# Kernel optimization log

Hardware: AMD Instinct MI355X
Metric: run time of the kernel (lower is better)

Reference implementation:

```python
import jax, jax.numpy as jnp
import numpy as np

PC = 512      # proposal_channels == conv_channels
INCH = 512    # in_channels of branch
B = 8
T = 64        # pyramid level length (feat_t) at order=0
TF = 256      # frame_level_feature length (clip_length)
KERNELS = [8, 16, 8, 4, 2, 2, 2]  # ConPoolingKernal
CLC = 498     # feature_lastclass channels (CLC + 2 == 500)
GROUPS = 32


def _gn(x, gamma, beta):
    # GroupNorm(32, C) over [B, C, L]
    Bb, C, L = x.shape
    xg = x.reshape(Bb, GROUPS, C // GROUPS, L)
    m = xg.mean(axis=(2, 3), keepdims=True)
    v = xg.var(axis=(2, 3), keepdims=True)
    xn = ((xg - m) * jax.lax.rsqrt(v + 1e-5)).reshape(Bb, C, L)
    return xn * gamma[None, :, None] + beta[None, :, None]


def _c1(x, w, b):
    # Unit1D kernel_shape=1: pointwise conv
    return jnp.einsum('bct,oc->bot', x, w) + b[None, :, None]


def _bmp(feat, segs):
    # BoundaryMaxPooling: first C/2 channels max-pooled over segs[...,0:2],
    # second C/2 over segs[...,2:4] (inclusive integer ranges, clamped).
    Bb, C, L = feat.shape
    C2 = C // 2
    pos = jnp.arange(L)
    def pool(f, s, e):
        s = jnp.clip(s, 0, L - 1)
        e = jnp.maximum(jnp.clip(e, 0, L - 1), s)
        mask = (pos[None, None, :] >= s[..., None]) & (pos[None, None, :] <= e[..., None])  # [B,T,L]
        return jnp.max(jnp.where(mask[:, None], f[:, :, None, :], -jnp.inf), axis=-1)  # [B,C2,T]
    return jnp.concatenate([pool(feat[:, :C2], segs[..., 0], segs[..., 1]),
                            pool(feat[:, C2:], segs[..., 2], segs[..., 3])], axis=1)


def _anchor_gather(feat, anc, K):
    # Vectorized per-anchor clamp/slice + nearest F.interpolate(size=K):
    # src index for output k of a slice [l, r] is l + floor(k * (r - l + 1) / K).
    Bb, C, L = feat.shape
    left = jnp.clip(anc[..., 0], 0, L)
    right = jnp.clip(anc[..., 1], 0, L)
    valid = right > left                      # empty slices -> zeros (torch branch)
    seglen = right + 1 - left
    k = jnp.arange(K)
    idx = jnp.clip(left[..., None] + (k[None, None, :] * seglen[..., None]) // K, 0, L - 1)  # [B,T,K]
    g = jax.vmap(lambda f, ix: f[:, ix])(feat, idx)   # [B,C,T,K]
    return g * valid[:, None, :, None].astype(feat.dtype)


def setup_inputs() -> dict:
    key = jax.random.key(0)
    ks = jax.random.split(key, 16)
    f32 = jnp.float32
    s = 0.02
    def w(k, shape):
        return jax.random.normal(k, shape, f32) * s
    inp = {}
    inp['feature'] = jax.random.normal(ks[0], (B, INCH, T), f32)
    inp['frame_level_feature'] = jax.random.normal(ks[1], (B, PC, TF), f32)
    inp['segments'] = jax.random.randint(ks[2], (B, T, 4), 0, T).astype(jnp.int32)
    inp['frame_segments'] = jax.random.randint(ks[3], (B, T, 4), 0, TF).astype(jnp.int32)
    inp['feature_lastclass'] = jax.random.normal(ks[4], (B, CLC, T), f32)
    inp['anchor'] = jnp.sort(jax.random.randint(ks[5], (B, T, 2), 0, T), axis=-1).astype(jnp.int32)
    inp['frame_anchor'] = jnp.sort(jax.random.randint(ks[6], (B, T, 2), 0, TF), axis=-1).astype(jnp.int32)
    inp['order'] = 0
    inp['LocResult_feature'] = jax.random.normal(ks[7], (B, 2, T), f32)
    inp['w_cur'] = w(ks[8], (PC, INCH)); inp['b_cur'] = jnp.zeros((PC,), f32)
    inp['g_cur'] = jnp.ones((PC,), f32); inp['be_cur'] = jnp.zeros((PC,), f32)
    inp['w_lr'] = w(ks[9], (2 * PC, INCH)); inp['b_lr'] = jnp.zeros((2 * PC,), f32)
    inp['g_lr'] = jnp.ones((2 * PC,), f32); inp['be_lr'] = jnp.zeros((2 * PC,), f32)
    inp['w_roi'] = w(ks[10], (PC, PC)); inp['b_roi'] = jnp.zeros((PC,), f32)
    inp['g_roi'] = jnp.ones((PC,), f32); inp['be_roi'] = jnp.zeros((PC,), f32)
    K1 = KERNELS[1]; K0 = KERNELS[0]
    inp['w_cp'] = w(ks[11], (PC, 2 * PC, K1)); inp['b_cp'] = jnp.zeros((PC,), f32)
    inp['w_cp0'] = w(ks[12], (PC, PC, K0)); inp['b_cp0'] = jnp.zeros((PC,), f32)
    CIN = 6 * PC + 500
    inp['w_prop'] = w(ks[13], (INCH, CIN)); inp['b_prop'] = jnp.zeros((INCH,), f32)
    inp['g_prop'] = jnp.ones((INCH,), f32); inp['be_prop'] = jnp.zeros((INCH,), f32)
    return inp


def reference(feature, frame_level_feature, segments, frame_segments, feature_lastclass,
              anchor, frame_anchor, order, LocResult_feature,
              w_cur, b_cur, g_cur, be_cur, w_lr, b_lr, g_lr, be_lr,
              w_roi, b_roi, g_roi, be_roi, w_cp, b_cp, w_cp0, b_cp0,
              w_prop, b_prop, g_prop, be_prop):
    relu = jax.nn.relu
    fm_short = relu(_gn(_c1(feature, w_cur, b_cur), g_cur, be_cur))           # [B,PC,T]
    feat_lr = relu(_gn(_c1(feature, w_lr, b_lr), g_lr, be_lr))                # [B,2PC,T]
    prop_feature = _bmp(feat_lr, segments)                                    # [B,2PC,T]
    prop_roi = relu(_gn(_c1(_bmp(frame_level_feature, frame_segments), w_roi, b_roi), g_roi, be_roi))
    K1 = KERNELS[order + 1]
    K0 = KERNELS[0]
    g1 = _anchor_gather(feat_lr, anchor, K1)                                  # [B,2PC,T,K1]
    con_feature = jnp.einsum('bctk,ock->bot', g1, w_cp) + b_cp[None, :, None]  # valid conv K1->1
    g0 = _anchor_gather(frame_level_feature, frame_anchor, K0)                # [B,PC,T,K0]
    frame_con = jnp.einsum('bctk,ock->bot', g0, w_cp0) + b_cp0[None, :, None]
    prop_con = relu(_gn(_c1(frame_con, w_roi, b_roi), g_roi, be_roi))
    cat = jnp.concatenate([prop_roi, prop_feature, fm_short, feature_lastclass,
                           con_feature, prop_con, LocResult_feature], axis=1)  # [B,6PC+500,T]
    out = relu(_gn(_c1(cat, w_prop, b_prop), g_prop, be_prop))                # [B,INCH,T]
    return (out, feat_lr)
```

## Files before the change

kernel.cpp:

```cpp
#include <hip/hip_runtime.h>
#include <math.h>

#define BB 8
#define CATP 3584
#define CAT_REAL 3572

typedef __attribute__((ext_vector_type(8))) short short8;
typedef __attribute__((ext_vector_type(4))) float f32x4;

__device__ inline ushort f2bf(float f) {
  union { float f; unsigned u; } x;
  x.f = f;
  return (ushort)((x.u + 0x7FFFu + ((x.u >> 16) & 1u)) >> 16);
}
__device__ inline float bf2f(unsigned us) {
  union { unsigned u; float f; } x;
  x.u = us << 16;
  return x.f;
}

template <int Cin, int Kf>
__device__ void cpT_tile(const float* __restrict__ W, ushort* __restrict__ D,
                         int nt, int cc) {
  const int tid = threadIdx.x;
  const int j = tid >> 6, l4 = (tid >> 4) & 3, l15 = tid & 15;
  const int o = nt * 64 + j * 16 + l15;
  const int cb = cc * 32 + l4 * 8;
  ushort rg[8][Kf];
#pragma unroll
  for (int q = 0; q < 8; q++) {
    const float* row = W + ((size_t)o * Cin + cb + q) * Kf;
#pragma unroll
    for (int kq = 0; kq < Kf / 4; kq++) {
      const float4 f = *(const float4*)(row + kq * 4);
      rg[q][kq * 4 + 0] = f2bf(f.x);
      rg[q][kq * 4 + 1] = f2bf(f.y);
      rg[q][kq * 4 + 2] = f2bf(f.z);
      rg[q][kq * 4 + 3] = f2bf(f.w);
    }
  }
#pragma unroll
  for (int k = 0; k < Kf; k++) {
    uint4 pk;
    pk.x = (unsigned)rg[0][k] | ((unsigned)rg[1][k] << 16);
    pk.y = (unsigned)rg[2][k] | ((unsigned)rg[3][k] << 16);
    pk.z = (unsigned)rg[4][k] | ((unsigned)rg[5][k] << 16);
    pk.w = (unsigned)rg[6][k] | ((unsigned)rg[7][k] << 16);
    *(uint4*)(D + ((size_t)(nt * Kf + k) * (Cin >> 5) + cc) * 2048 + tid * 8) = pk;
  }
}

__global__ __launch_bounds__(256) void prep_kernel(
    const float* __restrict__ w_cur, const float* __restrict__ w_lr,
    const float* __restrict__ w_roi, const float* __restrict__ w_prop,
    ushort* __restrict__ Wcomb, ushort* __restrict__ Wroi,
    ushort* __restrict__ Wprop, const float* __restrict__ w_cp,
    ushort* __restrict__ WcpT, const float* __restrict__ w_cp0,
    ushort* __restrict__ Wcp0T, const float* __restrict__ feature,
    const float* __restrict__ frame_feat, const float* __restrict__ lastcls,
    const float* __restrict__ locres, ushort* __restrict__ Ft,
    ushort* __restrict__ FfT, ushort* __restrict__ cat) {
  __shared__ float tile[64 * 65];
  const int bid = blockIdx.x;
  if (bid < 1408) {
    const int i = bid * 256 + threadIdx.x;
    const float* src;
    ushort* dst;
    int o, k8, Kc;
    bool pad = false;
    if (i < 98304) {
      o = i >> 6; k8 = i & 63; Kc = 16;
      src = (o < 512) ? (w_cur + (size_t)o * 512)
                      : (w_lr + (size_t)(o - 512) * 512);
      dst = Wcomb;
    } else if (i < 131072) {
      const int r = i - 98304;
      o = r >> 6; k8 = r & 63; Kc = 16;
      src = w_roi + (size_t)o * 512;
      dst = Wroi;
    } else {
      const int r = i - 131072;
      if (r >= 229376) return;
      o = r / 448; k8 = r % 448; Kc = 112;
      src = w_prop + (size_t)o * CAT_REAL;
      dst = Wprop;
      pad = true;
    }
    const int k = k8 * 8;
    float v[8];
    if (pad) {
#pragma unroll
      for (int q = 0; q < 8; q++) v[q] = (k + q < CAT_REAL) ? src[k + q] : 0.f;
    } else {
      const float4 f0 = *(const float4*)(src + k);
      const float4 f1 = *(const float4*)(src + k + 4);
      v[0] = f0.x; v[1] = f0.y; v[2] = f0.z; v[3] = f0.w;
      v[4] = f1.x; v[5] = f1.y; v[6] = f1.z; v[7] = f1.w;
    }
    uint4 pk;
    pk.x = (unsigned)f2bf(v[0]) | ((unsigned)f2bf(v[1]) << 16);
    pk.y = (unsigned)f2bf(v[2]) | ((unsigned)f2bf(v[3]) << 16);
    pk.z = (unsigned)f2bf(v[4]) | ((unsigned)f2bf(v[5]) << 16);
    pk.w = (unsigned)f2bf(v[6]) | ((unsigned)f2bf(v[7]) << 16);
    const int ot = o >> 6, ii = (o >> 4) & 3, l15 = o & 15;
    const int kc = k8 >> 2, l4 = k8 & 3;
    const size_t flat =
        ((((size_t)ot * Kc + kc) * 4 + ii) * 64 + l4 * 16 + l15) * 8;
    *(uint4*)(dst + flat) = pk;
    return;
  }
  if (bid < 1792) {
    const int local = bid - 1408;
    if (local < 256)
      cpT_tile<1024, 16>(w_cp, WcpT, local >> 5, local & 31);
    else {
      const int r = local - 256;
      cpT_tile<512, 8>(w_cp0, Wcp0T, r >> 4, r & 15);
    }
    return;
  }
  const int local = bid - 1792;
  const float* src;
  ushort* dst;
  int Cr, Cw, L, rs, co, cblk, lblk, b;
  if (local < 64) {
    src = feature; dst = Ft; Cr = 512; Cw = 512; L = 64; rs = 512; co = 0;
    cblk = local & 7; lblk = 0; b = local >> 3;
  } else if (local < 320) {
    const int r = local - 64;
    src = frame_feat; dst = FfT; Cr = 512; Cw = 512; L = 256; rs = 512; co = 0;
    cblk = r & 7; lblk = (r >> 3) & 3; b = r >> 5;
  } else if (local < 384) {
    const int r = local - 320;
    src = lastcls; dst = cat; Cr = 498; Cw = 498; L = 64; rs = CATP; co = 2048;
    cblk = r & 7; lblk = 0; b = r >> 3;
  } else {
    const int r = local - 384;
    src = locres; dst = cat; Cr = 2; Cw = 14; L = 64; rs = CATP; co = 3570;
    cblk = 0; lblk = 0; b = r;
  }
  const int c0 = cblk * 64, l0 = lblk * 64;
  for (int e = threadIdx.x; e < 4096; e += 256) {
    const int cc = e >> 6, ll = e & 63;
    const int c = c0 + cc;
    tile[cc * 65 + ll] = (c < Cr) ? src[((size_t)b * Cr + c) * L + l0 + ll] : 0.f;
  }
  __syncthreads();
  for (int e = threadIdx.x; e < 4096; e += 256) {
    const int ll = e >> 6, cc = e & 63;
    const int c = c0 + cc;
    if (c < Cw)
      dst[((size_t)b * L + l0 + ll) * rs + co + c] = f2bf(tile[cc * 65 + ll]);
  }
}

__global__ __launch_bounds__(256) void gemm_gn_seg_kernel(
    int nblk0,
    const ushort* __restrict__ X0, const ushort* __restrict__ W0,
    const float* __restrict__ b0, const float* __restrict__ g0,
    const float* __restrict__ e0, int Kp0, int cs0, float* of0, int om0,
    ushort* co0, int cst0, int coff0,
    const ushort* __restrict__ X1, const ushort* __restrict__ W1,
    const float* __restrict__ b1, const float* __restrict__ g1,
    const float* __restrict__ e1, int Kp1, int cs1, float* of1, int om1,
    ushort* co1, int cst1, int coff1) {
  const int bx = blockIdx.x;
  const bool s1 = bx >= nblk0;
  const ushort* Xt = s1 ? X1 : X0;
  const ushort* Wb = s1 ? W1 : W0;
  const float* bias = s1 ? b1 : b0;
  const float* gamma = s1 ? g1 : g0;
  const float* beta = s1 ? e1 : e0;
  const int Kp = s1 ? Kp1 : Kp0;
  const int cpgShift = s1 ? cs1 : cs0;
  float* outF = s1 ? of1 : of0;
  const int outFM = s1 ? om1 : om0;
  ushort* catOut = s1 ? co1 : co0;
  const int catStride = s1 ? cst1 : cst0;
  const int chOff = s1 ? coff1 : coff0;
  const int o0 = (s1 ? bx - nblk0 : bx) * 64;

  const int b = blockIdx.y;
  const int w = threadIdx.x >> 6;
  const int lane = threadIdx.x & 63;
  const int l15 = lane & 15, l4 = lane >> 4;
  const int wk = Kp >> 2;
  const int kbeg = w * wk, kend = kbeg + wk;

  f32x4 acc[4][4] = {};
  const ushort* wbase = Wb + (size_t)(o0 >> 6) * (Kp >> 5) * 2048 + lane * 8;
  const ushort* bp[4];
#pragma unroll
  for (int j = 0; j < 4; j++)
    bp[j] = Xt + (size_t)(b * 64 + j * 16 + l15) * Kp + l4 * 8;

  for (int k = kbeg; k < kend; k += 32) {
    const int kc = k >> 5;
    short8 a[4], x[4];
#pragma unroll
    for (int i = 0; i < 4; i++)
      a[i] = *(const short8*)(wbase + ((size_t)kc * 4 + i) * 512);
#pragma unroll
    for (int j = 0; j < 4; j++) x[j] = *(const short8*)(bp[j] + k);
#pragma unroll
    for (int i = 0; i < 4; i++)
#pragma unroll
      for (int j = 0; j < 4; j++)
        acc[i][j] = __builtin_amdgcn_mfma_f32_16x16x32_bf16(a[i], x[j],
                                                            acc[i][j], 0, 0, 0);
  }

  __shared__ float red[64 * 65];
  for (int ww = 0; ww < 4; ww++) {
    __syncthreads();
    if (w == ww) {
#pragma unroll
      for (int i = 0; i < 4; i++)
#pragma unroll
        for (int j = 0; j < 4; j++)
#pragma unroll
          for (int r = 0; r < 4; r++) {
            const int m = i * 16 + l4 * 4 + r;
            const int n = j * 16 + l15;
            if (ww == 0)
              red[m * 65 + n] = acc[i][j][r] + bias[o0 + m];
            else
              red[m * 65 + n] += acc[i][j][r];
          }
    }
  }
  __syncthreads();

  const int cpg = 1 << cpgShift;
  const int ngroups = 64 >> cpgShift;
  __shared__ float rs[4], rss[4], gmean[4], grstd[4];
  for (int gi = 0; gi < ngroups; gi++) {
    float s = 0.f, ss = 0.f;
    const int nel = cpg << 6;
    for (int e = threadIdx.x; e < nel; e += 256) {
      const float v = red[((gi << cpgShift) + (e >> 6)) * 65 + (e & 63)];
      s += v;
      ss += v * v;
    }
#pragma unroll
    for (int off = 32; off > 0; off >>= 1) {
      s += __shfl_down(s, off);
      ss += __shfl_down(ss, off);
    }
    if (lane == 0) { rs[w] = s; rss[w] = ss; }
    __syncthreads();
    if (threadIdx.x == 0) {
      const float ts = rs[0] + rs[1] + rs[2] + rs[3];
      const float tss = rss[0] + rss[1] + rss[2] + rss[3];
      const float mean = ts / (float)nel;
      const float var = tss / (float)nel - mean * mean;
      gmean[gi] = mean;
      grstd[gi] = rsqrtf(var + 1e-5f);
    }
    __syncthreads();
  }

  if (outF) {
    for (int e = threadIdx.x; e < 4096; e += 256) {
      const int m = e >> 6, n = e & 63;
      const int gi = m >> cpgShift;
      const int c = o0 + m;
      float v = (red[m * 65 + n] - gmean[gi]) * grstd[gi] * gamma[c] + beta[c];
      v = fmaxf(v, 0.f);
      outF[((size_t)b * outFM + c) * 64 + n] = v;
    }
  }
  if (catOut) {
    for (int e = threadIdx.x; e < 4096; e += 256) {
      const int n = e >> 6, m = e & 63;
      const int gi = m >> cpgShift;
      const int c = o0 + m;
      float v = (red[m * 65 + n] - gmean[gi]) * grstd[gi] * gamma[c] + beta[c];
      v = fmaxf(v, 0.f);
      catOut[((size_t)(b * 64) + n) * catStride + chOff + c] = f2bf(v);
    }
  }
}

__global__ __launch_bounds__(256) void gemm_part_kernel(
    const ushort* __restrict__ Xt, const ushort* __restrict__ Wb,
    float* __restrict__ P) {
  const int ot = blockIdx.x;
  const int b = blockIdx.y;
  const int kz = blockIdx.z;
  const int w = threadIdx.x >> 6;
  const int lane = threadIdx.x & 63;
  const int l15 = lane & 15, l4 = lane >> 4;
  const int kbeg = kz * 896 + w * 224;
  const int kend = kbeg + 224;

  f32x4 acc[4][4] = {};
  const ushort* wbase = Wb + (size_t)ot * (CATP >> 5) * 2048 + lane * 8;
  const ushort* bp[4];
#pragma unroll
  for (int j = 0; j < 4; j++)
    bp[j] = Xt + (size_t)(b * 64 + j * 16 + l15) * CATP + l4 * 8;

  for (int k = kbeg; k < kend; k += 32) {
    const int kc = k >> 5;
    short8 a[4], x[4];
#pragma unroll
    for (int i = 0; i < 4; i++)
      a[i] = *(const short8*)(wbase + ((size_t)kc * 4 + i) * 512);
#pragma unroll
    for (int j = 0; j < 4; j++) x[j] = *(const short8*)(bp[j] + k);
#pragma unroll
    for (int i = 0; i < 4; i++)
#pragma unroll
      for (int j = 0; j < 4; j++)
        acc[i][j] = __builtin_amdgcn_mfma_f32_16x16x32_bf16(a[i], x[j],
                                                            acc[i][j], 0, 0, 0);
  }

  __shared__ float red[64 * 65];
  for (int ww = 0; ww < 4; ww++) {
    __syncthreads();
    if (w == ww) {
#pragma unroll
      for (int i = 0; i < 4; i++)
#pragma unroll
        for (int j = 0; j < 4; j++)
#pragma unroll
          for (int r = 0; r < 4; r++) {
            const int m = i * 16 + l4 * 4 + r;
            const int n = j * 16 + l15;
            if (ww == 0)
              red[m * 65 + n] = acc[i][j][r];
            else
              red[m * 65 + n] += acc[i][j][r];
          }
    }
  }
  __syncthreads();
  float* Pp = P + (((size_t)kz * BB + b) * 512 + ot * 64) * 64;
  for (int e = threadIdx.x; e < 4096; e += 256) Pp[e] = red[(e >> 6) * 65 + (e & 63)];
}

__global__ __launch_bounds__(256) void reduce_gn_kernel(
    const float* __restrict__ P, const float* __restrict__ bias,
    const float* __restrict__ gamma, const float* __restrict__ beta,
    float* __restrict__ outF) {
  const int ot = blockIdx.x;
  const int b = blockIdx.y;
  const int o0 = ot * 64;
  const int w = threadIdx.x >> 6;
  const int lane = threadIdx.x & 63;
  __shared__ float red[64 * 65];
  for (int e = threadIdx.x; e < 4096; e += 256) {
    const int m = e >> 6, n = e & 63;
    float s = bias[o0 + m];
#pragma unroll
    for (int z = 0; z < 4; z++)
      s += P[(((size_t)z * BB + b) * 512 + o0 + m) * 64 + n];
    red[m * 65 + n] = s;
  }
  __syncthreads();
  __shared__ float rs[4], rss[4], gmean[4], grstd[4];
  for (int gi = 0; gi < 4; gi++) {
    float s = 0.f, ss = 0.f;
    for (int e = threadIdx.x; e < 1024; e += 256) {
      const float v = red[((gi << 4) + (e >> 6)) * 65 + (e & 63)];
      s += v;
      ss += v * v;
    }
#pragma unroll
    for (int off = 32; off > 0; off >>= 1) {
      s += __shfl_down(s, off);
      ss += __shfl_down(ss, off);
    }
    if (lane == 0) { rs[w] = s; rss[w] = ss; }
    __syncthreads();
    if (threadIdx.x == 0) {
      const float ts = rs[0] + rs[1] + rs[2] + rs[3];
      const float tss = rss[0] + rss[1] + rss[2] + rss[3];
      const float mean = ts / 1024.f;
      const float var = tss / 1024.f - mean * mean;
      gmean[gi] = mean;
      grstd[gi] = rsqrtf(var + 1e-5f);
    }
    __syncthreads();
  }
  for (int e = threadIdx.x; e < 4096; e += 256) {
    const int m = e >> 6, n = e & 63;
    const int gi = m >> 4;
    const int c = o0 + m;
    float v = (red[m * 65 + n] - gmean[gi]) * grstd[gi] * gamma[c] + beta[c];
    outF[((size_t)b * 512 + c) * 64 + n] = fmaxf(v, 0.f);
  }
}

template <int C, int L>
__device__ void bmp_body(const ushort* __restrict__ Xt,
                         const int* __restrict__ segs, ushort* __restrict__ Y,
                         int rowStride, int chOff, float2 (*pmax)[512]) {
  constexpr int C2 = C / 2;
  constexpr int P2 = C2 / 2;
  constexpr int CH = P2 / 64;
  const int t = blockIdx.x;
  const int b = blockIdx.y;
  const int w = threadIdx.x >> 6;
  const int lane = threadIdx.x & 63;
  const int* sg = segs + ((size_t)b * 64 + t) * 4;
  const ushort* Xb = Xt + (size_t)b * L * C;
#pragma unroll
  for (int h = 0; h < 2; h++) {
    const int s = min(max(sg[2 * h], 0), L - 1);
    const int e = max(min(max(sg[2 * h + 1], 0), L - 1), s);
#pragma unroll
    for (int q = 0; q < CH; q++) {
      const int p = q * 64 + lane;
      const ushort* base = Xb + h * C2 + 2 * p;
      float a0 = -INFINITY, a1 = -INFINITY;
      float c0 = -INFINITY, c1 = -INFINITY;
      int l = s + w;
      for (; l + 4 <= e; l += 8) {
        const unsigned u0 = *(const unsigned*)(base + (size_t)l * C);
        const unsigned u1 = *(const unsigned*)(base + (size_t)(l + 4) * C);
        a0 = fmaxf(a0, bf2f(u0 & 0xffffu));
        a1 = fmaxf(a1, bf2f(u0 >> 16));
        c0 = fmaxf(c0, bf2f(u1 & 0xffffu));
        c1 = fmaxf(c1, bf2f(u1 >> 16));
      }
      if (l <= e) {
        const unsigned u0 = *(const unsigned*)(base + (size_t)l * C);
        a0 = fmaxf(a0, bf2f(u0 & 0xffffu));
        a1 = fmaxf(a1, bf2f(u0 >> 16));
      }
      pmax[w][h * P2 + p] = make_float2(fmaxf(a0, c0), fmaxf(a1, c1));
    }
  }
  __syncthreads();
  for (int idx = threadIdx.x; idx < 2 * P2; idx += 256) {
    float2 m = pmax[0][idx];
#pragma unroll
    for (int ww = 1; ww < 4; ww++) {
      const float2 v = pmax[ww][idx];
      m.x = fmaxf(m.x, v.x);
      m.y = fmaxf(m.y, v.y);
    }
    const unsigned o = (unsigned)f2bf(m.x) | ((unsigned)f2bf(m.y) << 16);
    *(unsigned*)(Y + ((size_t)(b * 64) + t) * rowStride + chOff + 2 * idx) = o;
  }
}

__global__ __launch_bounds__(256) void bmp_dual_kernel(
    const ushort* __restrict__ FlrT, const int* __restrict__ segments,
    ushort* __restrict__ cat, const ushort* __restrict__ FfT,
    const int* __restrict__ frame_segs, ushort* __restrict__ XbmpT) {
  __shared__ float2 pm[4][512];
  if (blockIdx.z == 0)
    bmp_body<1024, 64>(FlrT, segments, cat, CATP, 512, pm);
  else
    bmp_body<512, 256>(FfT, frame_segs, XbmpT, 512, 0, pm);
}

template <int Kf, int L, int Cin>
__device__ void anchor_mfma_body(const ushort* __restrict__ src,
                                 const int* __restrict__ anc,
                                 const ushort* __restrict__ Wt,
                                 float* __restrict__ P, int slice, float* red) {
  const int nt = blockIdx.x;
  const int b = blockIdx.y;
  const int w = threadIdx.x >> 6;
  const int lane = threadIdx.x & 63;
  const int l15 = lane & 15, l4 = lane >> 4;
  const int kz = slice >> 1, chalf = slice & 1;
  const int k = kz * 4 + w;
  const int cbase = chalf * (Cin / 2);

  const ushort* rp[4];
#pragma unroll
  for (int i = 0; i < 4; i++) {
    const int t = i * 16 + l15;
    const int a0 = anc[((size_t)b * 64 + t) * 2 + 0];
    const int a1 = anc[((size_t)b * 64 + t) * 2 + 1];
    const int left = min(max(a0, 0), L);
    const int right = min(max(a1, 0), L);
    const int seglen = right + 1 - left;
    const int ix = min(max(left + (k * seglen) / Kf, 0), L - 1);
    rp[i] = src + ((size_t)b * L + ix) * Cin + cbase + l4 * 8;
  }
  const ushort* wb = Wt + (size_t)(nt * Kf + k) * (Cin >> 5) * 2048 + lane * 8;

  f32x4 acc[4][4] = {};
  for (int c0 = 0; c0 < Cin / 2; c0 += 32) {
    const int cc = (cbase + c0) >> 5;
    short8 a[4], bb[4];
#pragma unroll
    for (int i = 0; i < 4; i++) a[i] = *(const short8*)(rp[i] + c0);
#pragma unroll
    for (int j = 0; j < 4; j++)
      bb[j] = *(const short8*)(wb + ((size_t)cc * 4 + j) * 512);
#pragma unroll
    for (int i = 0; i < 4; i++)
#pragma unroll
      for (int j = 0; j < 4; j++)
        acc[i][j] = __builtin_amdgcn_mfma_f32_16x16x32_bf16(a[i], bb[j],
                                                            acc[i][j], 0, 0, 0);
  }

  for (int ww = 0; ww < 4; ww++) {
    __syncthreads();
    if (w == ww) {
#pragma unroll
      for (int i = 0; i < 4; i++)
#pragma unroll
        for (int j = 0; j < 4; j++)
#pragma unroll
          for (int r = 0; r < 4; r++) {
            const int m = i * 16 + l4 * 4 + r;
            const int n = j * 16 + l15;
            if (ww == 0)
              red[m * 65 + n] = acc[i][j][r];
            else
              red[m * 65 + n] += acc[i][j][r];
          }
    }
  }
  __syncthreads();
  float* Pp = P + (((size_t)slice * BB + b) * 512 + nt * 64) * 64;
  for (int e = threadIdx.x; e < 4096; e += 256) {
    const int n = e >> 6, m = e & 63;
    Pp[e] = red[m * 65 + n];
  }
}

__global__ __launch_bounds__(256) void anchor_mfma_dual_kernel(
    const ushort* __restrict__ FlrT, const int* __restrict__ anchor,
    const ushort* __restrict__ WcpT, float* __restrict__ P1,
    const ushort* __restrict__ FfT, const int* __restrict__ frame_anchor,
    const ushort* __restrict__ Wcp0T, float* __restrict__ P0) {
  __shared__ float red[64 * 65];
  const int z = blockIdx.z;
  if (z < 8)
    anchor_mfma_body<16, 64, 1024>(FlrT, anchor, WcpT, P1, z, red);
  else
    anchor_mfma_body<8, 256, 512>(FfT, frame_anchor, Wcp0T, P0, z - 8, red);
}

__device__ void anchor_reduce_body(const float* __restrict__ P, int ks,
                                   const float* __restrict__ bias,
                                   const int* __restrict__ anc, int L,
                                   ushort* __restrict__ Y, int rowStride,
                                   int chOff, float* tile, float* sval) {
  const int o0 = blockIdx.x * 64;
  const int b = blockIdx.y;
  if (threadIdx.x < 64) {
    const int t = threadIdx.x;
    const int a0 = anc[((size_t)b * 64 + t) * 2 + 0];
    const int a1 = anc[((size_t)b * 64 + t) * 2 + 1];
    const int left = min(max(a0, 0), L);
    const int right = min(max(a1, 0), L);
    sval[t] = (right > left) ? 1.f : 0.f;
  }
  __syncthreads();
  for (int e = threadIdx.x; e < 4096; e += 256) {
    const int nl = e >> 6, m = e & 63;
    const int n = o0 + nl;
    float s = 0.f;
    for (int z = 0; z < ks; z++)
      s += P[(((size_t)z * BB + b) * 512 + n) * 64 + m];
    tile[nl * 65 + m] = s * sval[m] + bias[n];
  }
  __syncthreads();
  for (int e = threadIdx.x; e < 4096; e += 256) {
    const int m = e >> 6, nl = e & 63;
    Y[((size_t)(b * 64) + m) * rowStride + chOff + o0 + nl] =
        f2bf(tile[nl * 65 + m]);
  }
}

__global__ __launch_bounds__(256) void anchor_reduce_dual_kernel(
    const float* __restrict__ P1, const float* __restrict__ b_cp,
    const int* __restrict__ anchor, ushort* __restrict__ cat,
    const float* __restrict__ P0, const float* __restrict__ b_cp0,
    const int* __restrict__ frame_anchor, ushort* __restrict__ FconT) {
  __shared__ float tile[64 * 65];
  __shared__ float sval[64];
  if (blockIdx.z == 0)
    anchor_reduce_body(P1, 8, b_cp, anchor, 64, cat, CATP, 2546, tile, sval);
  else
    anchor_reduce_body(P0, 4, b_cp0, frame_anchor, 256, FconT, 512, 0, tile, sval);
}

extern "C" void kernel_launch(void* const* d_in, const int* in_sizes, int n_in,
                              void* d_out, int out_size, void* d_ws,
                              size_t ws_size, hipStream_t stream) {
  const float* feature      = (const float*)d_in[0];
  const float* frame_feat   = (const float*)d_in[1];
  const int*   segments     = (const int*)d_in[2];
  const int*   frame_segs   = (const int*)d_in[3];
  const float* feat_lastcls = (const float*)d_in[4];
  const int*   anchor       = (const int*)d_in[5];
  const int*   frame_anchor = (const int*)d_in[6];
  const float* locres       = (const float*)d_in[8];
  const float* w_cur  = (const float*)d_in[9];
  const float* b_cur  = (const float*)d_in[10];
  const float* g_cur  = (const float*)d_in[11];
  const float* be_cur = (const float*)d_in[12];
  const float* w_lr   = (const float*)d_in[13];
  const float* b_lr   = (const float*)d_in[14];
  const float* g_lr   = (const float*)d_in[15];
  const float* be_lr  = (const float*)d_in[16];
  const float* w_roi  = (const float*)d_in[17];
  const float* b_roi  = (const float*)d_in[18];
  const float* g_roi  = (const float*)d_in[19];
  const float* be_roi = (const float*)d_in[20];
  const float* w_cp   = (const float*)d_in[21];
  const float* b_cp   = (const float*)d_in[22];
  const float* w_cp0  = (const float*)d_in[23];
  const float* b_cp0  = (const float*)d_in[24];
  const float* w_prop = (const float*)d_in[25];
  const float* b_prop = (const float*)d_in[26];
  const float* g_prop = (const float*)d_in[27];
  const float* be_prop= (const float*)d_in[28];

  float* out_main = (float*)d_out;
  float* feat_lr  = (float*)d_out + BB * 512 * 64;

  ushort* cat_t  = (ushort*)d_ws;
  ushort* Ft     = cat_t + 1835008;
  ushort* XbmpT  = Ft + 262144;
  ushort* FconT  = XbmpT + 262144;
  ushort* Wcomb  = FconT + 262144;
  ushort* Wroi   = Wcomb + 786432;
  ushort* Wprop  = Wroi + 262144;
  ushort* WcpT   = Wprop + 1835008;
  ushort* Wcp0T  = WcpT + 8388608;
  ushort* FlrT   = Wcp0T + 2097152;
  ushort* FfT    = FlrT + 524288;
  float*  P1     = (float*)(FfT + 1048576);
  float*  P0     = P1 + 2097152;
  float*  P9     = P0 + 1048576;

  prep_kernel<<<2184, 256, 0, stream>>>(
      w_cur, w_lr, w_roi, w_prop, Wcomb, Wroi, Wprop, w_cp, WcpT, w_cp0,
      Wcp0T, feature, frame_feat, feat_lastcls, locres, Ft, FfT, cat_t);

  gemm_gn_seg_kernel<<<dim3(24, BB), 256, 0, stream>>>(
      8,
      Ft, Wcomb, b_cur, g_cur, be_cur, 512, 4, nullptr, 0, cat_t, CATP, 1536,
      Ft, Wcomb + 512 * 512, b_lr, g_lr, be_lr, 512, 5, feat_lr, 1024, FlrT,
      1024, 0);

  bmp_dual_kernel<<<dim3(64, BB, 2), 256, 0, stream>>>(
      FlrT, segments, cat_t, FfT, frame_segs, XbmpT);

  anchor_mfma_dual_kernel<<<dim3(8, BB, 12), 256, 0, stream>>>(
      FlrT, anchor, WcpT, P1, FfT, frame_anchor, Wcp0T, P0);

  anchor_reduce_dual_kernel<<<dim3(8, BB, 2), 256, 0, stream>>>(
      P1, b_cp, anchor, cat_t, P0, b_cp0, frame_anchor, FconT);

  gemm_gn_seg_kernel<<<dim3(16, BB), 256, 0, stream>>>(
      8,
      XbmpT, Wroi, b_roi, g_roi, be_roi, 512, 4, nullptr, 0, cat_t, CATP, 0,
      FconT, Wroi, b_roi, g_roi, be_roi, 512, 4, nullptr, 0, cat_t, CATP, 3058);

  gemm_part_kernel<<<dim3(8, BB, 4), 256, 0, stream>>>(cat_t, Wprop, P9);

  reduce_gn_kernel<<<dim3(8, BB), 256, 0, stream>>>(
      P9, b_prop, g_prop, be_prop, out_main);
}
```

Baseline: 271.3 us.

## Regroup pipeline stages into dependency-ordered fused kernels with per-wave output tiling

```diff
diff --git a/kernel.cpp b/kernel.cpp
--- a/kernel.cpp
+++ b/kernel.cpp
@@ -154,86 +154,51 @@
   }
 }
 
-__global__ __launch_bounds__(256) void gemm_gn_seg_kernel(
-    int nblk0,
-    const ushort* __restrict__ X0, const ushort* __restrict__ W0,
-    const float* __restrict__ b0, const float* __restrict__ g0,
-    const float* __restrict__ e0, int Kp0, int cs0, float* of0, int om0,
-    ushort* co0, int cst0, int coff0,
-    const ushort* __restrict__ X1, const ushort* __restrict__ W1,
-    const float* __restrict__ b1, const float* __restrict__ g1,
-    const float* __restrict__ e1, int Kp1, int cs1, float* of1, int om1,
-    ushort* co1, int cst1, int coff1) {
-  const int bx = blockIdx.x;
-  const bool s1 = bx >= nblk0;
-  const ushort* Xt = s1 ? X1 : X0;
-  const ushort* Wb = s1 ? W1 : W0;
-  const float* bias = s1 ? b1 : b0;
-  const float* gamma = s1 ? g1 : g0;
-  const float* beta = s1 ? e1 : e0;
-  const int Kp = s1 ? Kp1 : Kp0;
-  const int cpgShift = s1 ? cs1 : cs0;
-  float* outF = s1 ? of1 : of0;
-  const int outFM = s1 ? om1 : om0;
-  ushort* catOut = s1 ? co1 : co0;
-  const int catStride = s1 ? cst1 : cst0;
-  const int chOff = s1 ? coff1 : coff0;
-  const int o0 = (s1 ? bx - nblk0 : bx) * 64;
-
-  const int b = blockIdx.y;
+__device__ void gemm_gn_body(const ushort* __restrict__ Xt,
+                             const ushort* __restrict__ Wb,
+                             const float* __restrict__ bias,
+                             const float* __restrict__ gamma,
+                             const float* __restrict__ beta, int Kp,
+                             int cpgShift, float* __restrict__ outF, int outFM,
+                             ushort* __restrict__ catOut, int catStride,
+                             int chOff, int ot, int b, float* smem) {
+  float* red = smem;
+  float* rs = smem + 4224;
+  float* rss = smem + 4228;
+  float* gmean = smem + 4232;
+  float* grstd = smem + 4236;
   const int w = threadIdx.x >> 6;
   const int lane = threadIdx.x & 63;
   const int l15 = lane & 15, l4 = lane >> 4;
-  const int wk = Kp >> 2;
-  const int kbeg = w * wk, kend = kbeg + wk;
-
-  f32x4 acc[4][4] = {};
-  const ushort* wbase = Wb + (size_t)(o0 >> 6) * (Kp >> 5) * 2048 + lane * 8;
+  const int o0 = ot * 64;
+
+  f32x4 acc[4] = {};
+  const ushort* wbase = Wb + (size_t)ot * (Kp >> 5) * 2048 + lane * 8;
   const ushort* bp[4];
 #pragma unroll
   for (int j = 0; j < 4; j++)
     bp[j] = Xt + (size_t)(b * 64 + j * 16 + l15) * Kp + l4 * 8;
-
-  for (int k = kbeg; k < kend; k += 32) {
-    const int kc = k >> 5;
-    short8 a[4], x[4];
-#pragma unroll
-    for (int i = 0; i < 4; i++)
-      a[i] = *(const short8*)(wbase + ((size_t)kc * 4 + i) * 512);
-#pragma unroll
-    for (int j = 0; j < 4; j++) x[j] = *(const short8*)(bp[j] + k);
-#pragma unroll
-    for (int i = 0; i < 4; i++)
-#pragma unroll
-      for (int j = 0; j < 4; j++)
-        acc[i][j] = __builtin_amdgcn_mfma_f32_16x16x32_bf16(a[i], x[j],
-                                                            acc[i][j], 0, 0, 0);
-  }
-
-  __shared__ float red[64 * 65];
-  for (int ww = 0; ww < 4; ww++) {
-    __syncthreads();
-    if (w == ww) {
-#pragma unroll
-      for (int i = 0; i < 4; i++)
-#pragma unroll
-        for (int j = 0; j < 4; j++)
-#pragma unroll
-          for (int r = 0; r < 4; r++) {
-            const int m = i * 16 + l4 * 4 + r;
-            const int n = j * 16 + l15;
-            if (ww == 0)
-              red[m * 65 + n] = acc[i][j][r] + bias[o0 + m];
-            else
-              red[m * 65 + n] += acc[i][j][r];
-          }
-    }
-  }
+  const int nkc = Kp >> 5;
+  for (int kc = 0; kc < nkc; kc++) {
+    const short8 a = *(const short8*)(wbase + ((size_t)kc * 4 + w) * 512);
+    short8 x[4];
+#pragma unroll
+    for (int j = 0; j < 4; j++) x[j] = *(const short8*)(bp[j] + kc * 32);
+#pragma unroll
+    for (int j = 0; j < 4; j++)
+      acc[j] = __builtin_amdgcn_mfma_f32_16x16x32_bf16(a, x[j], acc[j], 0, 0, 0);
+  }
+#pragma unroll
+  for (int j = 0; j < 4; j++)
+#pragma unroll
+    for (int r = 0; r < 4; r++) {
+      const int m = w * 16 + l4 * 4 + r;
+      red[m * 65 + j * 16 + l15] = acc[j][r] + bias[o0 + m];
+    }
   __syncthreads();
 
   const int cpg = 1 << cpgShift;
   const int ngroups = 64 >> cpgShift;
-  __shared__ float rs[4], rss[4], gmean[4], grstd[4];
   for (int gi = 0; gi < ngroups; gi++) {
     float s = 0.f, ss = 0.f;
     const int nel = cpg << 6;
@@ -282,63 +247,35 @@
   }
 }
 
-__global__ __launch_bounds__(256) void gemm_part_kernel(
-    const ushort* __restrict__ Xt, const ushort* __restrict__ Wb,
-    float* __restrict__ P) {
-  const int ot = blockIdx.x;
-  const int b = blockIdx.y;
-  const int kz = blockIdx.z;
+__device__ void gemm_part_body(const ushort* __restrict__ Xt,
+                               const ushort* __restrict__ Wb,
+                               float* __restrict__ P, int ot, int b, int slice,
+                               int kbeg, int kend) {
   const int w = threadIdx.x >> 6;
   const int lane = threadIdx.x & 63;
   const int l15 = lane & 15, l4 = lane >> 4;
-  const int kbeg = kz * 896 + w * 224;
-  const int kend = kbeg + 224;
-
-  f32x4 acc[4][4] = {};
+  f32x4 acc[4] = {};
   const ushort* wbase = Wb + (size_t)ot * (CATP >> 5) * 2048 + lane * 8;
   const ushort* bp[4];
 #pragma unroll
   for (int j = 0; j < 4; j++)
     bp[j] = Xt + (size_t)(b * 64 + j * 16 + l15) * CATP + l4 * 8;
-
   for (int k = kbeg; k < kend; k += 32) {
     const int kc = k >> 5;
-    short8 a[4], x[4];
-#pragma unroll
-    for (int i = 0; i < 4; i++)
-      a[i] = *(const short8*)(wbase + ((size_t)kc * 4 + i) * 512);
+    const short8 a = *(const short8*)(wbase + ((size_t)kc * 4 + w) * 512);
+    short8 x[4];
 #pragma unroll
     for (int j = 0; j < 4; j++) x[j] = *(const short8*)(bp[j] + k);
 #pragma unroll
-    for (int i = 0; i < 4; i++)
-#pragma unroll
-      for (int j = 0; j < 4; j++)
-        acc[i][j] = __builtin_amdgcn_mfma_f32_16x16x32_bf16(a[i], x[j],
-                                                            acc[i][j], 0, 0, 0);
-  }
-
-  __shared__ float red[64 * 65];
-  for (int ww = 0; ww < 4; ww++) {
-    __syncthreads();
-    if (w == ww) {
-#pragma unroll
-      for (int i = 0; i < 4; i++)
-#pragma unroll
-        for (int j = 0; j < 4; j++)
-#pragma unroll
-          for (int r = 0; r < 4; r++) {
-            const int m = i * 16 + l4 * 4 + r;
-            const int n = j * 16 + l15;
-            if (ww == 0)
-              red[m * 65 + n] = acc[i][j][r];
-            else
-              red[m * 65 + n] += acc[i][j][r];
-          }
-    }
-  }
-  __syncthreads();
-  float* Pp = P + (((size_t)kz * BB + b) * 512 + ot * 64) * 64;
-  for (int e = threadIdx.x; e < 4096; e += 256) Pp[e] = red[(e >> 6) * 65 + (e & 63)];
+    for (int j = 0; j < 4; j++)
+      acc[j] = __builtin_amdgcn_mfma_f32_16x16x32_bf16(a, x[j], acc[j], 0, 0, 0);
+  }
+  float* Pp = P + (((size_t)slice * BB + b) * 512 + ot * 64) * 64;
+#pragma unroll
+  for (int j = 0; j < 4; j++)
+#pragma unroll
+    for (int r = 0; r < 4; r++)
+      Pp[(w * 16 + l4 * 4 + r) * 64 + j * 16 + l15] = acc[j][r];
 }
 
 __global__ __launch_bounds__(256) void reduce_gn_kernel(
@@ -397,12 +334,11 @@
 template <int C, int L>
 __device__ void bmp_body(const ushort* __restrict__ Xt,
                          const int* __restrict__ segs, ushort* __restrict__ Y,
-                         int rowStride, int chOff, float2 (*pmax)[512]) {
+                         int rowStride, int chOff, int t, int b,
+                         float2 (*pmax)[512]) {
   constexpr int C2 = C / 2;
   constexpr int P2 = C2 / 2;
   constexpr int CH = P2 / 64;
-  const int t = blockIdx.x;
-  const int b = blockIdx.y;
   const int w = threadIdx.x >> 6;
   const int lane = threadIdx.x & 63;
   const int* sg = segs + ((size_t)b * 64 + t) * 4;
@@ -448,108 +384,58 @@
   }
 }
 
-__global__ __launch_bounds__(256) void bmp_dual_kernel(
-    const ushort* __restrict__ FlrT, const int* __restrict__ segments,
-    ushort* __restrict__ cat, const ushort* __restrict__ FfT,
-    const int* __restrict__ frame_segs, ushort* __restrict__ XbmpT) {
-  __shared__ float2 pm[4][512];
-  if (blockIdx.z == 0)
-    bmp_body<1024, 64>(FlrT, segments, cat, CATP, 512, pm);
-  else
-    bmp_body<512, 256>(FfT, frame_segs, XbmpT, 512, 0, pm);
-}
-
-template <int Kf, int L, int Cin>
-__device__ void anchor_mfma_body(const ushort* __restrict__ src,
-                                 const int* __restrict__ anc,
-                                 const ushort* __restrict__ Wt,
-                                 float* __restrict__ P, int slice, float* red) {
-  const int nt = blockIdx.x;
-  const int b = blockIdx.y;
+template <int Kf, int L, int Cin, int NT>
+__device__ void anchor_body2(const ushort* __restrict__ src,
+                             const int* __restrict__ anc,
+                             const ushort* __restrict__ Wt,
+                             float* __restrict__ P, int nt, int b, int slice) {
   const int w = threadIdx.x >> 6;
   const int lane = threadIdx.x & 63;
   const int l15 = lane & 15, l4 = lane >> 4;
-  const int kz = slice >> 1, chalf = slice & 1;
-  const int k = kz * 4 + w;
-  const int cbase = chalf * (Cin / 2);
-
-  const ushort* rp[4];
-#pragma unroll
-  for (int i = 0; i < 4; i++) {
-    const int t = i * 16 + l15;
-    const int a0 = anc[((size_t)b * 64 + t) * 2 + 0];
-    const int a1 = anc[((size_t)b * 64 + t) * 2 + 1];
-    const int left = min(max(a0, 0), L);
-    const int right = min(max(a1, 0), L);
-    const int seglen = right + 1 - left;
+  const int t = w * 16 + l15;
+  const int a0 = anc[((size_t)b * 64 + t) * 2 + 0];
+  const int a1 = anc[((size_t)b * 64 + t) * 2 + 1];
+  const int left = min(max(a0, 0), L);
+  const int right = min(max(a1, 0), L);
+  const int seglen = right + 1 - left;
+
+  f32x4 acc[4] = {};
+#pragma unroll
+  for (int kt = 0; kt < NT; kt++) {
+    const int k = slice * NT + kt;
     const int ix = min(max(left + (k * seglen) / Kf, 0), L - 1);
-    rp[i] = src + ((size_t)b * L + ix) * Cin + cbase + l4 * 8;
-  }
-  const ushort* wb = Wt + (size_t)(nt * Kf + k) * (Cin >> 5) * 2048 + lane * 8;
-
-  f32x4 acc[4][4] = {};
-  for (int c0 = 0; c0 < Cin / 2; c0 += 32) {
-    const int cc = (cbase + c0) >> 5;
-    short8 a[4], bb[4];
-#pragma unroll
-    for (int i = 0; i < 4; i++) a[i] = *(const short8*)(rp[i] + c0);
-#pragma unroll
-    for (int j = 0; j < 4; j++)
-      bb[j] = *(const short8*)(wb + ((size_t)cc * 4 + j) * 512);
-#pragma unroll
-    for (int i = 0; i < 4; i++)
+    const ushort* rp = src + ((size_t)b * L + ix) * Cin + l4 * 8;
+    const ushort* wb = Wt + ((size_t)nt * Kf + k) * (Cin >> 5) * 2048 + lane * 8;
+#pragma unroll 4
+    for (int c0 = 0; c0 < Cin; c0 += 32) {
+      const int cc = c0 >> 5;
+      const short8 a = *(const short8*)(rp + c0);
+      short8 bbf[4];
 #pragma unroll
       for (int j = 0; j < 4; j++)
-        acc[i][j] = __builtin_amdgcn_mfma_f32_16x16x32_bf16(a[i], bb[j],
-                                                            acc[i][j], 0, 0, 0);
-  }
-
-  for (int ww = 0; ww < 4; ww++) {
-    __syncthreads();
-    if (w == ww) {
-#pragma unroll
-      for (int i = 0; i < 4; i++)
-#pragma unroll
-        for (int j = 0; j < 4; j++)
-#pragma unroll
-          for (int r = 0; r < 4; r++) {
-            const int m = i * 16 + l4 * 4 + r;
-            const int n = j * 16 + l15;
-            if (ww == 0)
-              red[m * 65 + n] = acc[i][j][r];
-            else
-              red[m * 65 + n] += acc[i][j][r];
-          }
-    }
-  }
-  __syncthreads();
-  float* Pp = P + (((size_t)slice * BB + b) * 512 + nt * 64) * 64;
-  for (int e = threadIdx.x; e < 4096; e += 256) {
-    const int n = e >> 6, m = e & 63;
-    Pp[e] = red[m * 65 + n];
-  }
-}
-
-__global__ __launch_bounds__(256) void anchor_mfma_dual_kernel(
-    const ushort* __restrict__ FlrT, const int* __restrict__ anchor,
-    const ushort* __restrict__ WcpT, float* __restrict__ P1,
-    const ushort* __restrict__ FfT, const int* __restrict__ frame_anchor,
-    const ushort* __restrict__ Wcp0T, float* __restrict__ P0) {
-  __shared__ float red[64 * 65];
-  const int z = blockIdx.z;
-  if (z < 8)
-    anchor_mfma_body<16, 64, 1024>(FlrT, anchor, WcpT, P1, z, red);
-  else
-    anchor_mfma_body<8, 256, 512>(FfT, frame_anchor, Wcp0T, P0, z - 8, red);
+        bbf[j] = *(const short8*)(wb + ((size_t)cc * 4 + j) * 512);
+#pragma unroll
+      for (int j = 0; j < 4; j++)
+        acc[j] =
+            __builtin_amdgcn_mfma_f32_16x16x32_bf16(a, bbf[j], acc[j], 0, 0, 0);
+    }
+  }
+  float* Pp = P + (((size_t)slice * BB + b) * 64) * 512 + nt * 64;
+#pragma unroll
+  for (int j = 0; j < 4; j++)
+#pragma unroll
+    for (int r = 0; r < 4; r++)
+      Pp[(size_t)(w * 16 + l4 * 4 + r) * 512 + j * 16 + l15] = acc[j][r];
 }
 
 __device__ void anchor_reduce_body(const float* __restrict__ P, int ks,
                                    const float* __restrict__ bias,
                                    const int* __restrict__ anc, int L,
                                    ushort* __restrict__ Y, int rowStride,
-                                   int chOff, float* tile, float* sval) {
-  const int o0 = blockIdx.x * 64;
-  const int b = blockIdx.y;
+                                   int chOff, int ot, int b, float* smem) {
+  float* tile = smem;
+  float* sval = smem + 4160;
+  const int o0 = ot * 64;
   if (threadIdx.x < 64) {
     const int t = threadIdx.x;
     const int a0 = anc[((size_t)b * 64 + t) * 2 + 0];
@@ -560,12 +446,11 @@
   }
   __syncthreads();
   for (int e = threadIdx.x; e < 4096; e += 256) {
-    const int nl = e >> 6, m = e & 63;
-    const int n = o0 + nl;
+    const int m = e >> 6, nl = e & 63;
     float s = 0.f;
     for (int z = 0; z < ks; z++)
-      s += P[(((size_t)z * BB + b) * 512 + n) * 64 + m];
-    tile[nl * 65 + m] = s * sval[m] + bias[n];
+      s += P[(((size_t)z * BB + b) * 64 + m) * 512 + o0 + nl];
+    tile[nl * 65 + m] = s * sval[m] + bias[o0 + nl];
   }
   __syncthreads();
   for (int e = threadIdx.x; e < 4096; e += 256) {
@@ -575,17 +460,96 @@
   }
 }
 
-__global__ __launch_bounds__(256) void anchor_reduce_dual_kernel(
-    const float* __restrict__ P1, const float* __restrict__ b_cp,
-    const int* __restrict__ anchor, ushort* __restrict__ cat,
+__global__ __launch_bounds__(256) void fused_B_kernel(
+    const ushort* __restrict__ Ft, const ushort* __restrict__ Wcomb,
+    const float* __restrict__ b_cur, const float* __restrict__ g_cur,
+    const float* __restrict__ be_cur, ushort* __restrict__ cat,
+    const float* __restrict__ b_lr, const float* __restrict__ g_lr,
+    const float* __restrict__ be_lr, float* __restrict__ feat_lr,
+    ushort* __restrict__ FlrT, const ushort* __restrict__ FfT,
+    const int* __restrict__ frame_segs, ushort* __restrict__ XbmpT,
+    const int* __restrict__ frame_anchor, const ushort* __restrict__ Wcp0T,
+    float* __restrict__ P0) {
+  __shared__ __align__(16) float smem[4240];
+  const int bid = blockIdx.x;
+  if (bid < 128) {
+    const int nt = bid & 7, b = (bid >> 3) & 7, slice = bid >> 6;
+    anchor_body2<8, 256, 512, 4>(FfT, frame_anchor, Wcp0T, P0, nt, b, slice);
+  } else if (bid < 320) {
+    const int r = bid - 128;
+    const int b = r / 24, ot24 = r % 24;
+    if (ot24 < 8)
+      gemm_gn_body(Ft, Wcomb, b_cur, g_cur, be_cur, 512, 4, nullptr, 0, cat,
+                   CATP, 1536, ot24, b, smem);
+    else
+      gemm_gn_body(Ft, Wcomb + 512 * 512, b_lr, g_lr, be_lr, 512, 5, feat_lr,
+                   1024, FlrT, 1024, 0, ot24 - 8, b, smem);
+  } else {
+    const int r = bid - 320;
+    bmp_body<512, 256>(FfT, frame_segs, XbmpT, 512, 0, r & 63, r >> 6,
+                       (float2(*)[512])smem);
+  }
+}
+
+__global__ __launch_bounds__(256) void fused_C_kernel(
+    const ushort* __restrict__ FlrT, const int* __restrict__ segments,
+    ushort* __restrict__ cat, const int* __restrict__ anchor,
+    const ushort* __restrict__ WcpT, float* __restrict__ P1,
     const float* __restrict__ P0, const float* __restrict__ b_cp0,
-    const int* __restrict__ frame_anchor, ushort* __restrict__ FconT) {
-  __shared__ float tile[64 * 65];
-  __shared__ float sval[64];
-  if (blockIdx.z == 0)
-    anchor_reduce_body(P1, 8, b_cp, anchor, 64, cat, CATP, 2546, tile, sval);
-  else
-    anchor_reduce_body(P0, 4, b_cp0, frame_anchor, 256, FconT, 512, 0, tile, sval);
+    const int* __restrict__ frame_anchor, ushort* __restrict__ FconT,
+    const ushort* __restrict__ XbmpT, const ushort* __restrict__ Wroi,
+    const float* __restrict__ b_roi, const float* __restrict__ g_roi,
+    const float* __restrict__ be_roi) {
+  __shared__ __align__(16) float smem[4240];
+  const int bid = blockIdx.x;
+  if (bid < 256) {
+    const int nt = bid & 7, b = (bid >> 3) & 7, slice = bid >> 6;
+    anchor_body2<16, 64, 1024, 4>(FlrT, anchor, WcpT, P1, nt, b, slice);
+  } else if (bid < 320) {
+    const int r = bid - 256;
+    gemm_gn_body(XbmpT, Wroi, b_roi, g_roi, be_roi, 512, 4, nullptr, 0, cat,
+                 CATP, 0, r & 7, r >> 3, smem);
+  } else if (bid < 384) {
+    const int r = bid - 320;
+    anchor_reduce_body(P0, 2, b_cp0, frame_anchor, 256, FconT, 512, 0, r & 7,
+                       r >> 3, smem);
+  } else {
+    const int r = bid - 384;
+    bmp_body<1024, 64>(FlrT, segments, cat, CATP, 512, r & 63, r >> 6,
+                       (float2(*)[512])smem);
+  }
+}
+
+__global__ __launch_bounds__(256) void fused_D_kernel(
+    const ushort* __restrict__ cat, const ushort* __restrict__ Wprop,
+    float* __restrict__ P9, const float* __restrict__ P1,
+    const float* __restrict__ b_cp, const int* __restrict__ anchor,
+    ushort* __restrict__ catw, const ushort* __restrict__ FconT,
+    const ushort* __restrict__ Wroi, const float* __restrict__ b_roi,
+    const float* __restrict__ g_roi, const float* __restrict__ be_roi) {
+  __shared__ __align__(16) float smem[4240];
+  const int bid = blockIdx.x;
+  if (bid < 192) {
+    const int s = bid >> 6, q = bid & 63;
+    const int kb = (s == 0) ? 0 : (s == 1) ? 864 : 1728;
+    const int ke = (s == 0) ? 864 : (s == 1) ? 1728 : 2528;
+    gemm_part_body(cat, Wprop, P9, q & 7, q >> 3, s, kb, ke);
+  } else if (bid < 256) {
+    const int r = bid - 192;
+    anchor_reduce_body(P1, 4, b_cp, anchor, 64, catw, CATP, 2546, r & 7,
+                       r >> 3, smem);
+  } else {
+    const int r = bid - 256;
+    gemm_gn_body(FconT, Wroi, b_roi, g_roi, be_roi, 512, 4, nullptr, 0, catw,
+                 CATP, 3058, r & 7, r >> 3, smem);
+  }
+}
+
+__global__ __launch_bounds__(256) void part_E_kernel(
+    const ushort* __restrict__ cat, const ushort* __restrict__ Wprop,
+    float* __restrict__ P9) {
+  gemm_part_body(cat, Wprop, P9, blockIdx.x & 7, blockIdx.x >> 3, 3, 2528,
+                 3584);
 }
 
 extern "C" void kernel_launch(void* const* d_in, const int* in_sizes, int n_in,
@@ -642,27 +606,19 @@
       w_cur, w_lr, w_roi, w_prop, Wcomb, Wroi, Wprop, w_cp, WcpT, w_cp0,
       Wcp0T, feature, frame_feat, feat_lastcls, locres, Ft, FfT, cat_t);
 
-  gemm_gn_seg_kernel<<<dim3(24, BB), 256, 0, stream>>>(
-      8,
-      Ft, Wcomb, b_cur, g_cur, be_cur, 512, 4, nullptr, 0, cat_t, CATP, 1536,
-      Ft, Wcomb + 512 * 512, b_lr, g_lr, be_lr, 512, 5, feat_lr, 1024, FlrT,
-      1024, 0);
-
-  bmp_dual_kernel<<<dim3(64, BB, 2), 256, 0, stream>>>(
-      FlrT, segments, cat_t, FfT, frame_segs, XbmpT);
-
-  anchor_mfma_dual_kernel<<<dim3(8, BB, 12), 256, 0, stream>>>(
-      FlrT, anchor, WcpT, P1, FfT, frame_anchor, Wcp0T, P0);
-
-  anchor_reduce_dual_kernel<<<dim3(8, BB, 2), 256, 0, stream>>>(
-      P1, b_cp, anchor, cat_t, P0, b_cp0, frame_anchor, FconT);
-
-  gemm_gn_seg_kernel<<<dim3(16, BB), 256, 0, stream>>>(
-      8,
-      XbmpT, Wroi, b_roi, g_roi, be_roi, 512, 4, nullptr, 0, cat_t, CATP, 0,
-      FconT, Wroi, b_roi, g_roi, be_roi, 512, 4, nullptr, 0, cat_t, CATP, 3058);
-
-  gemm_part_kernel<<<dim3(8, BB, 4), 256, 0, stream>>>(cat_t, Wprop, P9);
+  fused_B_kernel<<<832, 256, 0, stream>>>(
+      Ft, Wcomb, b_cur, g_cur, be_cur, cat_t, b_lr, g_lr, be_lr, feat_lr,
+      FlrT, FfT, frame_segs, XbmpT, frame_anchor, Wcp0T, P0);
+
+  fused_C_kernel<<<896, 256, 0, stream>>>(
+      FlrT, segments, cat_t, anchor, WcpT, P1, P0, b_cp0, frame_anchor, FconT,
+      XbmpT, Wroi, b_roi, g_roi, be_roi);
+
+  fused_D_kernel<<<320, 256, 0, stream>>>(
+      cat_t, Wprop, P9, P1, b_cp, anchor, cat_t, FconT, Wroi, b_roi, g_roi,
+      be_roi);
+
+  part_E_kernel<<<64, 256, 0, stream>>>(cat_t, Wprop, P9);
 
   reduce_gn_kernel<<<dim3(8, BB), 256, 0, stream>>>(
       P9, b_prop, g_prop, be_prop, out_main);
```

New measurement: 326.9 us. +20.5%, slower.
